# Kernel optimization log

Measured on AMD Instinct MI355X. Metric: run time of the kernel, lower is better.

Reference implementation:

```python
import jax, jax.numpy as jnp
import numpy as np

EMB = 64
L = 2
NU = 100000
NI = 50000
ER = 1000000
ET = 800000
EP = 200000


def setup_inputs() -> dict:
    key = jax.random.key(0)
    ks = jax.random.split(key, 32)
    f = jnp.float32
    def nrm(k, shape, s=0.01):
        return (jax.random.normal(k, shape) * s).astype(f)
    inp = {}
    # graph structure (int)
    inp['rate_src'] = jax.random.randint(ks[0], (ER,), 0, NU)
    inp['rate_dst'] = jax.random.randint(ks[1], (ER,), 0, NI)
    inp['trust_src'] = jax.random.randint(ks[2], (ET,), 0, NU)
    inp['trust_dst'] = jax.random.randint(ks[3], (ET,), 0, NU)
    inp['pos_u'] = jax.random.randint(ks[4], (EP,), 0, NU)
    inp['pos_i'] = jax.random.randint(ks[5], (EP,), 0, NI)
    inp['neg_u'] = jax.random.randint(ks[6], (EP,), 0, NU)
    inp['neg_i'] = jax.random.randint(ks[7], (EP,), 0, NI)
    # embeddings (init normal(0, 0.01) per init_weights)
    inp['eu'] = nrm(ks[8], (NU, EMB))
    inp['ei'] = nrm(ks[9], (NI, EMB))
    # per-rel GATv2 params, stacked over L layers; [:,0]=fc_src, [:,1]=fc_dst
    inp['rate_W'] = nrm(ks[10], (L, 2, EMB, EMB))
    inp['rate_b'] = jnp.zeros((L, 2, EMB), f)
    inp['rate_attn'] = nrm(ks[11], (L, EMB), 0.1)
    inp['rate_bias'] = jnp.zeros((L, EMB), f)
    inp['rb_W'] = nrm(ks[12], (L, 2, EMB, EMB))
    inp['rb_b'] = jnp.zeros((L, 2, EMB), f)
    inp['rb_attn'] = nrm(ks[13], (L, EMB), 0.1)
    inp['rb_bias'] = jnp.zeros((L, EMB), f)
    inp['tr_W'] = nrm(ks[14], (L, 2, EMB, EMB))
    inp['tr_b'] = jnp.zeros((L, 2, EMB), f)
    inp['tr_attn'] = nrm(ks[15], (L, EMB), 0.1)
    inp['tr_bias'] = jnp.zeros((L, EMB), f)
    # attention-gate MLPs: [:, 0]=influence, [:, 1]=interest
    inp['attW1'] = nrm(ks[16], (L, 2, 2 * EMB, 2 * EMB))
    inp['attb1'] = jnp.zeros((L, 2, 2 * EMB), f)
    inp['attW2'] = nrm(ks[17], (L, 2, 2 * EMB))
    inp['attb2'] = jnp.zeros((L, 2), f)
    return inp


def gatv2(hs, hd, src, dst, Ws, bs, Wd, bd, attn, bias, n_dst):
    # DGL GATv2Conv, num_heads=1: e = attn . leaky_relu(Ws h_u + Wd h_v), slope 0.2
    fs = hs @ Ws + bs          # [Ns, E]
    fd = hd @ Wd + bd          # [Nd, E]
    e = jax.nn.leaky_relu(fs[src] + fd[dst], 0.2) @ attn  # [E]
    m = jax.ops.segment_max(e, dst, num_segments=n_dst)
    ex = jnp.exp(e - m[dst])
    denom = jax.ops.segment_sum(ex, dst, num_segments=n_dst)
    alpha = ex / denom[dst]
    out = jax.ops.segment_sum(alpha[:, None] * fs[src], dst, num_segments=n_dst)
    return out + bias


def _bn1(x):
    # BatchNorm1d(1), training-mode batch stats, affine identity at init
    mu = jnp.mean(x)
    var = jnp.mean((x - mu) ** 2)
    return (x - mu) * jax.lax.rsqrt(var + 1e-5)


def reference(eu, ei, rate_W, rate_b, rate_attn, rate_bias, rb_W, rb_b, rb_attn,
              rb_bias, tr_W, tr_b, tr_attn, tr_bias, attW1, attb1, attW2, attb2,
              rate_src, rate_dst, trust_src, trust_dst, pos_u, pos_i, neg_u, neg_i):
    n_users, n_items = eu.shape[0], ei.shape[0]
    hu, hi = eu, ei
    res_u, res_i = [eu], [ei]
    for l in range(rate_W.shape[0]):
        # interest diffusion: rate (user->item) and rated-by (item->user, reverse edges)
        hi_new = gatv2(hu, hi, rate_src, rate_dst, rate_W[l, 0], rate_b[l, 0],
                       rate_W[l, 1], rate_b[l, 1], rate_attn[l], rate_bias[l], n_items) + hi
        q = gatv2(hi, hu, rate_dst, rate_src, rb_W[l, 0], rb_b[l, 0],
                  rb_W[l, 1], rb_b[l, 1], rb_attn[l], rb_bias[l], n_users)
        # influence diffusion: trust (user->user)
        p = gatv2(hu, hu, trust_src, trust_dst, tr_W[l, 0], tr_b[l, 0],
                  tr_W[l, 1], tr_b[l, 1], tr_attn[l], tr_bias[l], n_users)
        def att(h2, i):
            z = (h2 @ attW1[l, i] + attb1[l, i]) @ attW2[l, i] + attb2[l, i]  # [N]
            return jax.nn.leaky_relu(_bn1(z), 0.01)
        a_inf = att(jnp.concatenate([hu, p], axis=1), 0)
        a_int = att(jnp.concatenate([hu, q], axis=1), 1)
        gamma = jax.nn.softmax(jnp.stack([a_inf, a_int], axis=1), axis=1)  # [N,2]
        hu = gamma[:, 0:1] * p + gamma[:, 1:2] * q + hu
        hi = hi_new
        res_u.append(hu)
        res_i.append(hi)
    hu_all = jnp.concatenate(res_u, axis=1)  # [NU, EMB*(1+L)]
    hi_all = jnp.concatenate(res_i, axis=1)
    pos = jnp.sum(hu_all[pos_u] * hi_all[pos_i], axis=1, keepdims=True)  # [EP,1]
    neg = jnp.sum(hu_all[neg_u] * hi_all[neg_i], axis=1, keepdims=True)
    return pos, neg
```

## Files before the change

kernel.cpp:

```cpp
#include <hip/hip_runtime.h>
#include <hip/hip_bf16.h>
#include <cstdint>

typedef __hip_bfloat16 bf16;
typedef __attribute__((ext_vector_type(8))) short frag_ab;
typedef __attribute__((ext_vector_type(4))) float frag_cd;
typedef __attribute__((ext_vector_type(4))) short short4v;

__device__ __forceinline__ float b2f(short s){
  return __uint_as_float(((unsigned)(unsigned short)s) << 16);
}
__device__ __forceinline__ void bf_split(float x, short& hi, short& lo){
  bf16 h = __float2bfloat16(x);
  float hf = __bfloat162float(h);
  bf16 l = __float2bfloat16(x - hf);
  __builtin_memcpy(&hi, &h, 2);
  __builtin_memcpy(&lo, &l, 2);
}

__device__ __forceinline__ float wave_sum(float v){
#pragma unroll
  for (int o = 32; o > 0; o >>= 1) v += __shfl_down(v, o, 64);
  return v;
}

__global__ void k_copy_in(const float* __restrict__ src, float* __restrict__ dst,
                          int n, int stride){
  int idx = blockIdx.x * 256 + threadIdx.x;
  if (idx >= n * 64) return;
  int r = idx >> 6, j = idx & 63;
  dst[(size_t)r * stride + j] = src[idx];
}

__global__ void k_wsplit(const float* __restrict__ rateW, const float* __restrict__ rbW,
                         const float* __restrict__ trW,
                         short* __restrict__ Whi, short* __restrict__ Wlo){
  int tid = blockIdx.x * 256 + threadIdx.x;
  if (tid >= 12 * 4096) return;
  int m = tid >> 12, rem = tid & 4095;
  int lane = rem >> 6, rem2 = rem & 63;
  int pair = rem2 >> 3, j = rem2 & 7;
  int c = pair >> 1, h = pair & 1;
  int rel = m >> 2, li = m & 3;
  const float* base = (rel == 0) ? rateW : (rel == 1) ? rbW : trW;
  float v = base[(size_t)li * 4096 + (32 * h + (lane >> 4) * 8 + j) * 64 + 16 * c + (lane & 15)];
  short sh, sl; bf_split(v, sh, sl);
  Whi[tid] = sh; Wlo[tid] = sl;
}

__global__ void k_linear_multi(const float* __restrict__ x, int xs, int xo, int n,
                               const short* __restrict__ Whi, const short* __restrict__ Wlo,
                               int mcount,
                               int m0, const float* __restrict__ b0, bf16* __restrict__ o0,
                               int m1, const float* __restrict__ b1, bf16* __restrict__ o1,
                               int m2, const float* __restrict__ b2, bf16* __restrict__ o2,
                               int m3, const float* __restrict__ b3, bf16* __restrict__ o3){
  int lane = threadIdx.x & 63, w = threadIdx.x >> 6;
  int quad = lane >> 4, n16 = lane & 15;
  int rowbase = blockIdx.x * 64 + w * 16;
  if (rowbase >= n) return;
  int lrow = rowbase + n16; if (lrow >= n) lrow = n - 1;
  const float* xp = x + (size_t)lrow * xs + xo;
  frag_ab ahi[2], alo[2];
#pragma unroll
  for (int h = 0; h < 2; ++h){
    frag_ab vh, vl;
#pragma unroll
    for (int j = 0; j < 8; ++j){
      float xv = xp[32 * h + quad * 8 + j];
      short sh, sl; bf_split(xv, sh, sl);
      vh[j] = sh; vl[j] = sl;
    }
    ahi[h] = vh; alo[h] = vl;
  }
  int ms[4] = {m0, m1, m2, m3};
  const float* bs[4] = {b0, b1, b2, b3};
  bf16* os[4] = {o0, o1, o2, o3};
  for (int i = 0; i < mcount; ++i){
    const frag_ab* Bh = (const frag_ab*)(Whi + (size_t)ms[i] * 4096 + lane * 64);
    const frag_ab* Bl = (const frag_ab*)(Wlo + (size_t)ms[i] * 4096 + lane * 64);
    frag_cd acc[4];
#pragma unroll
    for (int c = 0; c < 4; ++c) acc[c] = frag_cd{0.f, 0.f, 0.f, 0.f};
#pragma unroll
    for (int c = 0; c < 4; ++c)
#pragma unroll
      for (int h = 0; h < 2; ++h){
        frag_ab bh = Bh[c * 2 + h], bl = Bl[c * 2 + h];
        acc[c] = __builtin_amdgcn_mfma_f32_16x16x32_bf16(ahi[h], bh, acc[c], 0, 0, 0);
        acc[c] = __builtin_amdgcn_mfma_f32_16x16x32_bf16(alo[h], bh, acc[c], 0, 0, 0);
        acc[c] = __builtin_amdgcn_mfma_f32_16x16x32_bf16(ahi[h], bl, acc[c], 0, 0, 0);
      }
    const float* bb = bs[i];
    bf16* oo = os[i];
#pragma unroll
    for (int reg = 0; reg < 4; ++reg){
      int r = rowbase + quad * 4 + reg;
      if (r >= n) continue;
#pragma unroll
      for (int c = 0; c < 4; ++c)
        oo[(size_t)r * 64 + 16 * c + n16] = __float2bfloat16(acc[c][reg] + bb[16 * c + n16]);
    }
  }
}

__global__ void k_hist2pos(const int* __restrict__ src, const int* __restrict__ dst,
                           int* __restrict__ cntA, int* __restrict__ cntB,
                           int* __restrict__ posA, int* __restrict__ posB, int E){
  int k = blockIdx.x * 256 + threadIdx.x;
  if (k >= E) return;
  posA[k] = atomicAdd(cntA + dst[k], 1);
  posB[k] = atomicAdd(cntB + src[k], 1);
}
__global__ void k_histpos(const int* __restrict__ dst, int* __restrict__ cnt,
                          int* __restrict__ pos, int E){
  int k = blockIdx.x * 256 + threadIdx.x;
  if (k >= E) return;
  pos[k] = atomicAdd(cnt + dst[k], 1);
}

__global__ void k_scan_mb(const int* __restrict__ cnt, int n,
                          int* __restrict__ offs, int* __restrict__ gbase){
  __shared__ int wsum[16];
  __shared__ int base_sh;
  int t = threadIdx.x, lane = t & 63, w = t >> 6;
  int i = blockIdx.x * 1024 + t;
  int v = (i < n) ? cnt[i] : 0;
  int x = v;
#pragma unroll
  for (int o = 1; o < 64; o <<= 1){
    int y = __shfl_up(x, o, 64);
    if (lane >= o) x += y;
  }
  if (lane == 63) wsum[w] = x;
  __syncthreads();
  if (t == 0){
    int tot = 0;
    for (int k = 0; k < 16; ++k){ int c = wsum[k]; wsum[k] = tot; tot += c; }
    base_sh = atomicAdd(gbase, tot);
  }
  __syncthreads();
  if (i < n) offs[i] = base_sh + wsum[w] + x - v;
}

__global__ void k_fill2_na(const int* __restrict__ src, const int* __restrict__ dst,
                           const int* __restrict__ offsA, const int* __restrict__ posA,
                           int* __restrict__ csrA,
                           const int* __restrict__ offsB, const int* __restrict__ posB,
                           int* __restrict__ csrB, int E){
  int t = blockIdx.x * 256 + threadIdx.x;
  int T = gridDim.x * 256;
  int k0 = t, k1 = t + T;
  bool b0 = k0 < E, b1 = k1 < E;
  int s0 = 0, d0 = 0, s1 = 0, d1 = 0, p0 = 0, q0 = 0, p1 = 0, q1 = 0;
  if (b0){ s0 = src[k0]; d0 = dst[k0]; p0 = posA[k0]; q0 = posB[k0]; }
  if (b1){ s1 = src[k1]; d1 = dst[k1]; p1 = posA[k1]; q1 = posB[k1]; }
  int oa0 = 0, ob0 = 0, oa1 = 0, ob1 = 0;
  if (b0){ oa0 = offsA[d0]; ob0 = offsB[s0]; }
  if (b1){ oa1 = offsA[d1]; ob1 = offsB[s1]; }
  if (b0){ csrA[oa0 + p0] = s0; csrB[ob0 + q0] = d0; }
  if (b1){ csrA[oa1 + p1] = s1; csrB[ob1 + q1] = d1; }
}
__global__ void k_fill_na(const int* __restrict__ src, const int* __restrict__ dst,
                          const int* __restrict__ offs, const int* __restrict__ pos,
                          int* __restrict__ csr, int E){
  int t = blockIdx.x * 256 + threadIdx.x;
  int T = gridDim.x * 256;
  int k0 = t, k1 = t + T;
  bool b0 = k0 < E, b1 = k1 < E;
  int s0 = 0, d0 = 0, p0 = 0, s1 = 0, d1 = 0, p1 = 0;
  if (b0){ s0 = src[k0]; d0 = dst[k0]; p0 = pos[k0]; }
  if (b1){ s1 = src[k1]; d1 = dst[k1]; p1 = pos[k1]; }
  int o0 = 0, o1 = 0;
  if (b0) o0 = offs[d0];
  if (b1) o1 = offs[d1];
  if (b0) csr[o0 + p0] = s0;
  if (b1) csr[o1 + p1] = s1;
}

__global__ void k_gat(const int* __restrict__ offs, const int* __restrict__ cnt,
                      const int* __restrict__ csr_src,
                      const bf16* __restrict__ fs, const bf16* __restrict__ fd,
                      const float* __restrict__ attn, const float* __restrict__ bias,
                      float* __restrict__ out, int os, int oo,
                      const float* __restrict__ res, int rs, int ro, int n){
  int d = blockIdx.x * 4 + (threadIdx.x >> 6);
  if (d >= n) return;
  int lane = threadIdx.x & 63;
  int g = lane >> 4, l16 = lane & 15;
  short4v dv = *(const short4v*)(fd + (size_t)d * 64 + 4 * l16);
  float fd0 = b2f(dv[0]), fd1 = b2f(dv[1]), fd2 = b2f(dv[2]), fd3 = b2f(dv[3]);
  float4 a4 = *(const float4*)(attn + 4 * l16);
  float acc0 = 0.f, acc1 = 0.f, acc2 = 0.f, acc3 = 0.f, den = 0.f;
  int idx0 = offs[d], end = idx0 + cnt[d];
  for (int idx = idx0; idx < end; idx += 4){
    int e = idx + g;
    bool valid = e < end;
    int s = csr_src[valid ? e : idx];
    short4v sv = *(const short4v*)(fs + (size_t)s * 64 + 4 * l16);
    float f0 = b2f(sv[0]), f1 = b2f(sv[1]), f2 = b2f(sv[2]), f3 = b2f(sv[3]);
    float v0 = f0 + fd0; v0 = (v0 > 0.f ? v0 : 0.2f * v0) * a4.x;
    float v1 = f1 + fd1; v1 = (v1 > 0.f ? v1 : 0.2f * v1) * a4.y;
    float v2 = f2 + fd2; v2 = (v2 > 0.f ? v2 : 0.2f * v2) * a4.z;
    float v3 = f3 + fd3; v3 = (v3 > 0.f ? v3 : 0.2f * v3) * a4.w;
    float tt = (v0 + v1) + (v2 + v3);
#pragma unroll
    for (int o = 1; o < 16; o <<= 1) tt += __shfl_xor(tt, o, 64);
    float ex = valid ? __expf(tt) : 0.f;
    acc0 += ex * f0; acc1 += ex * f1; acc2 += ex * f2; acc3 += ex * f3;
    den += ex;
  }
#pragma unroll
  for (int o = 16; o < 64; o <<= 1){
    acc0 += __shfl_xor(acc0, o, 64); acc1 += __shfl_xor(acc1, o, 64);
    acc2 += __shfl_xor(acc2, o, 64); acc3 += __shfl_xor(acc3, o, 64);
    den  += __shfl_xor(den, o, 64);
  }
  if (g == 0){
    float4 b4 = *(const float4*)(bias + 4 * l16);
    float inv = (den > 0.f) ? 1.f / den : 0.f;
    float o0 = acc0 * inv + b4.x, o1 = acc1 * inv + b4.y;
    float o2 = acc2 * inv + b4.z, o3 = acc3 * inv + b4.w;
    if (res){
      float4 r4 = *(const float4*)(res + (size_t)d * rs + ro + 4 * l16);
      o0 += r4.x; o1 += r4.y; o2 += r4.z; o3 += r4.w;
    }
    *(float4*)(out + (size_t)d * os + oo + 4 * l16) = make_float4(o0, o1, o2, o3);
  }
}

__global__ void k_attvec(const float* __restrict__ W1, const float* __restrict__ b1,
                         const float* __restrict__ W2, const float* __restrict__ b2,
                         float* __restrict__ vvec, float* __restrict__ cs){
  int t = threadIdx.x;
  int li = t >> 7, r = t & 127;
  float acc = 0.f;
  for (int c = 0; c < 128; ++c)
    acc += W1[(size_t)(li * 128 + r) * 128 + c] * W2[li * 128 + c];
  vvec[li * 128 + r] = acc;
  if (r == 0){
    float cacc = b2[li];
    for (int c = 0; c < 128; ++c)
      cacc += b1[li * 128 + c] * W2[li * 128 + c];
    cs[li] = cacc;
  }
}

__global__ void k_gate_z(const float* __restrict__ hu_all, int l,
                         const float* __restrict__ p, const float* __restrict__ q,
                         const float* __restrict__ vvec, const float* __restrict__ cs,
                         float* __restrict__ z1, float* __restrict__ z2,
                         float* __restrict__ bsums, int n){
  __shared__ float part[4][4];
  int w = threadIdx.x >> 6, j = threadIdx.x & 63;
  int nidx = blockIdx.x * 4 + w;
  float lz1 = 0.f, lz2 = 0.f;
  if (nidx < n){
    const float* v1 = vvec + l * 256;
    const float* v2 = vvec + l * 256 + 128;
    float h  = hu_all[(size_t)nidx * 192 + l * 64 + j];
    float pv = p[(size_t)nidx * 64 + j];
    float qv = q[(size_t)nidx * 64 + j];
    float t1 = wave_sum(h * v1[j] + pv * v1[64 + j]);
    float t2 = wave_sum(h * v2[j] + qv * v2[64 + j]);
    if (j == 0){
      lz1 = t1 + cs[l * 2 + 0];
      lz2 = t2 + cs[l * 2 + 1];
      z1[nidx] = lz1;
      z2[nidx] = lz2;
    }
  }
  if (j == 0){
    part[w][0] = lz1; part[w][1] = lz1 * lz1;
    part[w][2] = lz2; part[w][3] = lz2 * lz2;
  }
  __syncthreads();
  if (threadIdx.x < 4)
    bsums[(size_t)blockIdx.x * 4 + threadIdx.x] =
        part[0][threadIdx.x] + part[1][threadIdx.x] +
        part[2][threadIdx.x] + part[3][threadIdx.x];
}

__global__ void k_bn_part(const float* __restrict__ bsums, int nb,
                          double* __restrict__ gpart){
  __shared__ double sh[256];
  int c = threadIdx.x & 3, r0 = blockIdx.x * 64 + (threadIdx.x >> 2);
  double acc = 0.0;
  for (int i = r0; i < nb; i += gridDim.x * 64)
    acc += (double)bsums[(size_t)i * 4 + c];
  sh[threadIdx.x] = acc;
  __syncthreads();
  for (int s = 128; s >= 4; s >>= 1){
    if (threadIdx.x < s) sh[threadIdx.x] += sh[threadIdx.x + s];
    __syncthreads();
  }
  if (threadIdx.x < 4) gpart[(size_t)blockIdx.x * 4 + threadIdx.x] = sh[threadIdx.x];
}

__global__ void k_bn_final(const double* __restrict__ gpart, int nbk,
                           double* __restrict__ sums){
  __shared__ double sh[256];
  int c = threadIdx.x & 3, k0 = threadIdx.x >> 2;
  double acc = 0.0;
  for (int i = k0; i < nbk; i += 64) acc += gpart[(size_t)i * 4 + c];
  sh[threadIdx.x] = acc;
  __syncthreads();
  for (int s = 128; s >= 4; s >>= 1){
    if (threadIdx.x < s) sh[threadIdx.x] += sh[threadIdx.x + s];
    __syncthreads();
  }
  if (threadIdx.x < 4) sums[threadIdx.x] = sh[threadIdx.x];
}

__global__ void k_gate_combine(float* __restrict__ hu_all, int l,
                               const float* __restrict__ p, const float* __restrict__ q,
                               const float* __restrict__ z1, const float* __restrict__ z2,
                               const double* __restrict__ sums, int n){
  int idx = blockIdx.x * 256 + threadIdx.x;
  if (idx >= n * 64) return;
  int r = idx >> 6, j = idx & 63;
  double invn = 1.0 / (double)n;
  double mu1 = sums[0] * invn, mu2 = sums[2] * invn;
  float var1 = (float)(sums[1] * invn - mu1 * mu1);
  float var2 = (float)(sums[3] * invn - mu2 * mu2);
  float rs1 = rsqrtf(var1 + 1e-5f), rs2 = rsqrtf(var2 + 1e-5f);
  float a1 = (z1[r] - (float)mu1) * rs1;
  float a2 = (z2[r] - (float)mu2) * rs2;
  a1 = a1 > 0.f ? a1 : 0.01f * a1;
  a2 = a2 > 0.f ? a2 : 0.01f * a2;
  float mx = fmaxf(a1, a2);
  float e1 = __expf(a1 - mx), e2 = __expf(a2 - mx);
  float inv = 1.f / (e1 + e2);
  float out = (e1 * inv) * p[idx] + (e2 * inv) * q[idx]
            + hu_all[(size_t)r * 192 + l * 64 + j];
  hu_all[(size_t)r * 192 + (l + 1) * 64 + j] = out;
}

__global__ void k_score(const int* __restrict__ pu, const int* __restrict__ pi,
                        const int* __restrict__ nu, const int* __restrict__ ni,
                        const float* __restrict__ hu_all, const float* __restrict__ hi_all,
                        float* __restrict__ out, int EP){
  int gw = blockIdx.x * 4 + (threadIdx.x >> 6);
  int sub = (threadIdx.x >> 4) & 3, l16 = threadIdx.x & 15;
  int k = gw * 4 + sub;
  if (k >= 2 * EP) return;
  int u, i;
  if (k < EP){ u = pu[k]; i = pi[k]; } else { u = nu[k - EP]; i = ni[k - EP]; }
  const float4* hu = (const float4*)(hu_all + (size_t)u * 192);
  const float4* hi = (const float4*)(hi_all + (size_t)i * 192);
  float acc = 0.f;
#pragma unroll
  for (int t = 0; t < 3; ++t){
    float4 a = hu[l16 + 16 * t];
    float4 b = hi[l16 + 16 * t];
    acc += a.x * b.x + a.y * b.y + a.z * b.z + a.w * b.w;
  }
#pragma unroll
  for (int o = 8; o > 0; o >>= 1) acc += __shfl_xor(acc, o, 64);
  if (l16 == 0) out[k] = acc;
}

extern "C" void kernel_launch(void* const* d_in, const int* in_sizes, int n_in,
                              void* d_out, int out_size, void* d_ws, size_t ws_size,
                              hipStream_t stream) {
  const int*   rate_src  = (const int*)  d_in[0];
  const int*   rate_dst  = (const int*)  d_in[1];
  const int*   trust_src = (const int*)  d_in[2];
  const int*   trust_dst = (const int*)  d_in[3];
  const int*   pos_u     = (const int*)  d_in[4];
  const int*   pos_i     = (const int*)  d_in[5];
  const int*   neg_u     = (const int*)  d_in[6];
  const int*   neg_i     = (const int*)  d_in[7];
  const float* eu        = (const float*)d_in[8];
  const float* ei        = (const float*)d_in[9];
  const float* rate_W    = (const float*)d_in[10];
  const float* rate_b    = (const float*)d_in[11];
  const float* rate_attn = (const float*)d_in[12];
  const float* rate_bias = (const float*)d_in[13];
  const float* rb_W      = (const float*)d_in[14];
  const float* rb_b      = (const float*)d_in[15];
  const float* rb_attn   = (const float*)d_in[16];
  const float* rb_bias   = (const float*)d_in[17];
  const float* tr_W      = (const float*)d_in[18];
  const float* tr_b      = (const float*)d_in[19];
  const float* tr_attn   = (const float*)d_in[20];
  const float* tr_bias   = (const float*)d_in[21];
  const float* attW1     = (const float*)d_in[22];
  const float* attb1     = (const float*)d_in[23];
  const float* attW2     = (const float*)d_in[24];
  const float* attb2     = (const float*)d_in[25];

  const int ER = in_sizes[0];
  const int ET = in_sizes[2];
  const int EP = in_sizes[4];
  const int NU = in_sizes[8] / 64;
  const int NI = in_sizes[9] / 64;

  float* ws = (float*)d_ws;
  float*  hu_all = ws;
  float*  hi_all = hu_all + (size_t)NU * 192;
  float*  p      = hi_all + (size_t)NI * 192;
  float*  q      = p + (size_t)NU * 64;
  bf16*   tb     = (bf16*)(q + (size_t)NU * 64);
  bf16*   fsA    = tb;
  bf16*   fdB    = tb + (size_t)NU * 64;
  bf16*   fsC    = tb + (size_t)NU * 128;
  bf16*   fdC    = tb + (size_t)NU * 192;
  bf16*   fdA    = (bf16*)p;
  bf16*   fsB    = (bf16*)p + (size_t)NI * 64;
  int*    posA   = (int*)fsA;
  int*    posB   = (int*)fdB;
  int*    posC   = (int*)fsC;
  float*  z1     = (float*)(tb + (size_t)NU * 256);
  float*  z2     = z1 + NU;
  float*  bsums  = z2 + NU;
  float*  vvec   = bsums + (size_t)(((NU + 3) / 4) * 4);
  float*  cs     = vvec + 512;
  double* sums   = (double*)(((uintptr_t)(cs + 4) + 15) & ~(uintptr_t)15);
  double* gpart  = sums + 4;
  short*  Whi    = (short*)(gpart + 512);
  short*  Wlo    = Whi + 12 * 4096;
  int*    iw     = (int*)(Wlo + 12 * 4096);
  int*    cntA   = iw;
  int*    cntB   = cntA + NI;
  int*    cntC   = cntB + NU;
  int*    gbase  = cntC + NU;
  int*    offsA  = gbase + 4;
  int*    offsB  = offsA + NI;
  int*    offsC  = offsB + NU;
  int*    csrA   = offsC + NU;
  int*    csrB   = csrA + ER;
  int*    csrC   = csrB + ER;

  auto cdiv = [](int a, int b){ return (a + b - 1) / b; };
  const int nbz = cdiv(NU, 4);

  k_copy_in<<<cdiv(NU * 64, 256), 256, 0, stream>>>(eu, hu_all, NU, 192);
  k_copy_in<<<cdiv(NI * 64, 256), 256, 0, stream>>>(ei, hi_all, NI, 192);
  k_attvec<<<1, 512, 0, stream>>>(attW1, attb1, attW2, attb2, vvec, cs);
  k_wsplit<<<192, 256, 0, stream>>>(rate_W, rb_W, tr_W, Whi, Wlo);

  hipMemsetAsync(cntA, 0, (size_t)(NI + 2 * NU + 4) * 4, stream);
  k_hist2pos<<<cdiv(ER, 256), 256, 0, stream>>>(rate_src, rate_dst, cntA, cntB,
                                                posA, posB, ER);
  k_histpos<<<cdiv(ET, 256), 256, 0, stream>>>(trust_dst, cntC, posC, ET);
  k_scan_mb<<<cdiv(NI, 1024), 1024, 0, stream>>>(cntA, NI, offsA, gbase + 0);
  k_scan_mb<<<cdiv(NU, 1024), 1024, 0, stream>>>(cntB, NU, offsB, gbase + 1);
  k_scan_mb<<<cdiv(NU, 1024), 1024, 0, stream>>>(cntC, NU, offsC, gbase + 2);
  k_fill2_na<<<cdiv(ER, 512), 256, 0, stream>>>(rate_src, rate_dst,
      offsA, posA, csrA, offsB, posB, csrB, ER);
  k_fill_na<<<cdiv(ET, 512), 256, 0, stream>>>(trust_src, trust_dst,
      offsC, posC, csrC, ET);

  for (int l = 0; l < 2; ++l){
    k_linear_multi<<<cdiv(NU, 64), 256, 0, stream>>>(hu_all, 192, l * 64, NU, Whi, Wlo, 4,
        0 + l * 2 + 0, rate_b + (l * 2 + 0) * 64, fsA,
        4 + l * 2 + 1, rb_b   + (l * 2 + 1) * 64, fdB,
        8 + l * 2 + 0, tr_b   + (l * 2 + 0) * 64, fsC,
        8 + l * 2 + 1, tr_b   + (l * 2 + 1) * 64, fdC);
    k_linear_multi<<<cdiv(NI, 64), 256, 0, stream>>>(hi_all, 192, l * 64, NI, Whi, Wlo, 2,
        0 + l * 2 + 1, rate_b + (l * 2 + 1) * 64, fdA,
        4 + l * 2 + 0, rb_b   + (l * 2 + 0) * 64, fsB,
        0, (const float*)nullptr, (bf16*)nullptr,
        0, (const float*)nullptr, (bf16*)nullptr);

    k_gat<<<cdiv(NI, 4), 256, 0, stream>>>(offsA, cntA, csrA, fsA, fdA,
        rate_attn + l * 64, rate_bias + l * 64,
        hi_all, 192, (l + 1) * 64, hi_all, 192, l * 64, NI);
    k_gat<<<cdiv(NU, 4), 256, 0, stream>>>(offsB, cntB, csrB, fsB, fdB,
        rb_attn + l * 64, rb_bias + l * 64,
        q, 64, 0, (const float*)nullptr, 0, 0, NU);
    k_gat<<<cdiv(NU, 4), 256, 0, stream>>>(offsC, cntC, csrC, fsC, fdC,
        tr_attn + l * 64, tr_bias + l * 64,
        p, 64, 0, (const float*)nullptr, 0, 0, NU);

    k_gate_z<<<nbz, 256, 0, stream>>>(hu_all, l, p, q, vvec, cs, z1, z2, bsums, NU);
    k_bn_part<<<128, 256, 0, stream>>>(bsums, nbz, gpart);
    k_bn_final<<<1, 256, 0, stream>>>(gpart, 128, sums);
    k_gate_combine<<<cdiv(NU * 64, 256), 256, 0, stream>>>(hu_all, l, p, q, z1, z2, sums, NU);
  }

  k_score<<<cdiv(2 * EP, 16), 256, 0, stream>>>(pos_u, pos_i, neg_u, neg_i,
      hu_all, hi_all, (float*)d_out, EP);
}
```

Before: 1.001 ms.

## Add fp16 shadow embeddings for scoring, fuse graph build kernels, widen GAT lanes

Keeps fp16 copies of the user and item layer embeddings, written alongside the fp32 outputs, so the final scoring gather reads half the bytes. Merges the histogram and CSR fill kernels across relations, with positions stored as u16. Widens the GAT kernel to 8 lanes per edge with 16-byte loads, so 8 edges are processed per iteration. Risks fp16 precision loss in the scores, u16 overflow if a node's degree exceeds 65535, and needs extra workspace, falling back to fp32 when it is too small.

Measured after the change: 961.2 us. 4.0% less time.

```diff
diff --git a/kernel.cpp b/kernel.cpp
--- a/kernel.cpp
+++ b/kernel.cpp
@@ -1,14 +1,24 @@
 #include <hip/hip_runtime.h>
 #include <hip/hip_bf16.h>
+#include <hip/hip_fp16.h>
 #include <cstdint>
 
 typedef __hip_bfloat16 bf16;
 typedef __attribute__((ext_vector_type(8))) short frag_ab;
 typedef __attribute__((ext_vector_type(4))) float frag_cd;
 typedef __attribute__((ext_vector_type(4))) short short4v;
+typedef __attribute__((ext_vector_type(8))) short short8v;
+typedef unsigned short u16;
 
 __device__ __forceinline__ float b2f(short s){
   return __uint_as_float(((unsigned)(unsigned short)s) << 16);
+}
+__device__ __forceinline__ float h2f(short s){
+  __half h; __builtin_memcpy(&h, &s, 2); return __half2float(h);
+}
+__device__ __forceinline__ short f2h_s(float x){
+  __half h = __float2half(x);
+  short s; __builtin_memcpy(&s, &h, 2); return s;
 }
 __device__ __forceinline__ void bf_split(float x, short& hi, short& lo){
   bf16 h = __float2bfloat16(x);
@@ -24,12 +34,23 @@
   return v;
 }
 
-__global__ void k_copy_in(const float* __restrict__ src, float* __restrict__ dst,
-                          int n, int stride){
+__global__ void k_copy_in2(const float* __restrict__ eu, const float* __restrict__ ei,
+                           float* __restrict__ hu, float* __restrict__ hi,
+                           __half* __restrict__ huf, __half* __restrict__ hif,
+                           int NU, int NI){
   int idx = blockIdx.x * 256 + threadIdx.x;
-  if (idx >= n * 64) return;
-  int r = idx >> 6, j = idx & 63;
-  dst[(size_t)r * stride + j] = src[idx];
+  int tu = NU * 16;
+  if (idx >= tu + NI * 16) return;
+  const float* srcp; float* dstp; __half* fp_; int r, jj;
+  if (idx < tu){ r = idx >> 4; jj = idx & 15; srcp = eu; dstp = hu; fp_ = huf; }
+  else { int t = idx - tu; r = t >> 4; jj = t & 15; srcp = ei; dstp = hi; fp_ = hif; }
+  float4 v = *(const float4*)(srcp + (size_t)r * 64 + 4 * jj);
+  *(float4*)(dstp + (size_t)r * 192 + 4 * jj) = v;
+  if (fp_){
+    short4v h;
+    h[0] = f2h_s(v.x); h[1] = f2h_s(v.y); h[2] = f2h_s(v.z); h[3] = f2h_s(v.w);
+    *(short4v*)((short*)fp_ + (size_t)r * 192 + 4 * jj) = h;
+  }
 }
 
 __global__ void k_wsplit(const float* __restrict__ rateW, const float* __restrict__ rbW,
@@ -104,19 +125,21 @@
   }
 }
 
-__global__ void k_hist2pos(const int* __restrict__ src, const int* __restrict__ dst,
+__global__ void k_hist_all(const int* __restrict__ rate_src, const int* __restrict__ rate_dst,
+                           const int* __restrict__ trust_dst,
                            int* __restrict__ cntA, int* __restrict__ cntB,
-                           int* __restrict__ posA, int* __restrict__ posB, int E){
+                           int* __restrict__ cntC,
+                           u16* __restrict__ posA, u16* __restrict__ posB,
+                           u16* __restrict__ posC, int ER, int ET){
   int k = blockIdx.x * 256 + threadIdx.x;
-  if (k >= E) return;
-  posA[k] = atomicAdd(cntA + dst[k], 1);
-  posB[k] = atomicAdd(cntB + src[k], 1);
-}
-__global__ void k_histpos(const int* __restrict__ dst, int* __restrict__ cnt,
-                          int* __restrict__ pos, int E){
-  int k = blockIdx.x * 256 + threadIdx.x;
-  if (k >= E) return;
-  pos[k] = atomicAdd(cnt + dst[k], 1);
+  if (k < ER){
+    int d = rate_dst[k], s = rate_src[k];
+    posA[k] = (u16)atomicAdd(cntA + d, 1);
+    posB[k] = (u16)atomicAdd(cntB + s, 1);
+  }
+  if (k < ET){
+    posC[k] = (u16)atomicAdd(cntC + trust_dst[k], 1);
+  }
 }
 
 __global__ void k_scan_mb(const int* __restrict__ cnt, int n,
@@ -143,39 +166,24 @@
   if (i < n) offs[i] = base_sh + wsum[w] + x - v;
 }
 
-__global__ void k_fill2_na(const int* __restrict__ src, const int* __restrict__ dst,
-                           const int* __restrict__ offsA, const int* __restrict__ posA,
+__global__ void k_fill_all(const int* __restrict__ rate_src, const int* __restrict__ rate_dst,
+                           const int* __restrict__ trust_src, const int* __restrict__ trust_dst,
+                           const int* __restrict__ offsA, const u16* __restrict__ posA,
                            int* __restrict__ csrA,
-                           const int* __restrict__ offsB, const int* __restrict__ posB,
-                           int* __restrict__ csrB, int E){
-  int t = blockIdx.x * 256 + threadIdx.x;
-  int T = gridDim.x * 256;
-  int k0 = t, k1 = t + T;
-  bool b0 = k0 < E, b1 = k1 < E;
-  int s0 = 0, d0 = 0, s1 = 0, d1 = 0, p0 = 0, q0 = 0, p1 = 0, q1 = 0;
-  if (b0){ s0 = src[k0]; d0 = dst[k0]; p0 = posA[k0]; q0 = posB[k0]; }
-  if (b1){ s1 = src[k1]; d1 = dst[k1]; p1 = posA[k1]; q1 = posB[k1]; }
-  int oa0 = 0, ob0 = 0, oa1 = 0, ob1 = 0;
-  if (b0){ oa0 = offsA[d0]; ob0 = offsB[s0]; }
-  if (b1){ oa1 = offsA[d1]; ob1 = offsB[s1]; }
-  if (b0){ csrA[oa0 + p0] = s0; csrB[ob0 + q0] = d0; }
-  if (b1){ csrA[oa1 + p1] = s1; csrB[ob1 + q1] = d1; }
-}
-__global__ void k_fill_na(const int* __restrict__ src, const int* __restrict__ dst,
-                          const int* __restrict__ offs, const int* __restrict__ pos,
-                          int* __restrict__ csr, int E){
-  int t = blockIdx.x * 256 + threadIdx.x;
-  int T = gridDim.x * 256;
-  int k0 = t, k1 = t + T;
-  bool b0 = k0 < E, b1 = k1 < E;
-  int s0 = 0, d0 = 0, p0 = 0, s1 = 0, d1 = 0, p1 = 0;
-  if (b0){ s0 = src[k0]; d0 = dst[k0]; p0 = pos[k0]; }
-  if (b1){ s1 = src[k1]; d1 = dst[k1]; p1 = pos[k1]; }
-  int o0 = 0, o1 = 0;
-  if (b0) o0 = offs[d0];
-  if (b1) o1 = offs[d1];
-  if (b0) csr[o0 + p0] = s0;
-  if (b1) csr[o1 + p1] = s1;
+                           const int* __restrict__ offsB, const u16* __restrict__ posB,
+                           int* __restrict__ csrB,
+                           const int* __restrict__ offsC, const u16* __restrict__ posC,
+                           int* __restrict__ csrC, int ER, int ET){
+  int k = blockIdx.x * 256 + threadIdx.x;
+  if (k < ER){
+    int s = rate_src[k], d = rate_dst[k];
+    csrA[offsA[d] + (int)posA[k]] = s;
+    csrB[offsB[s] + (int)posB[k]] = d;
+  }
+  if (k < ET){
+    int s = trust_src[k], d = trust_dst[k];
+    csrC[offsC[d] + (int)posC[k]] = s;
+  }
 }
 
 __global__ void k_gat(const int* __restrict__ offs, const int* __restrict__ cnt,
@@ -183,49 +191,74 @@
                       const bf16* __restrict__ fs, const bf16* __restrict__ fd,
                       const float* __restrict__ attn, const float* __restrict__ bias,
                       float* __restrict__ out, int os, int oo,
-                      const float* __restrict__ res, int rs, int ro, int n){
+                      const float* __restrict__ res, int rs, int ro,
+                      __half* __restrict__ fout, int n){
   int d = blockIdx.x * 4 + (threadIdx.x >> 6);
   if (d >= n) return;
   int lane = threadIdx.x & 63;
-  int g = lane >> 4, l16 = lane & 15;
-  short4v dv = *(const short4v*)(fd + (size_t)d * 64 + 4 * l16);
-  float fd0 = b2f(dv[0]), fd1 = b2f(dv[1]), fd2 = b2f(dv[2]), fd3 = b2f(dv[3]);
-  float4 a4 = *(const float4*)(attn + 4 * l16);
-  float acc0 = 0.f, acc1 = 0.f, acc2 = 0.f, acc3 = 0.f, den = 0.f;
+  int g = lane >> 3, l8 = lane & 7;
+  short8v dv = *(const short8v*)(fd + (size_t)d * 64 + 8 * l8);
+  float fdv[8];
+#pragma unroll
+  for (int j = 0; j < 8; ++j) fdv[j] = b2f(dv[j]);
+  float4 a0 = *(const float4*)(attn + 8 * l8);
+  float4 a1 = *(const float4*)(attn + 8 * l8 + 4);
+  float a8[8] = {a0.x, a0.y, a0.z, a0.w, a1.x, a1.y, a1.z, a1.w};
+  float acc[8];
+#pragma unroll
+  for (int j = 0; j < 8; ++j) acc[j] = 0.f;
+  float den = 0.f;
   int idx0 = offs[d], end = idx0 + cnt[d];
-  for (int idx = idx0; idx < end; idx += 4){
+  for (int idx = idx0; idx < end; idx += 8){
     int e = idx + g;
     bool valid = e < end;
     int s = csr_src[valid ? e : idx];
-    short4v sv = *(const short4v*)(fs + (size_t)s * 64 + 4 * l16);
-    float f0 = b2f(sv[0]), f1 = b2f(sv[1]), f2 = b2f(sv[2]), f3 = b2f(sv[3]);
-    float v0 = f0 + fd0; v0 = (v0 > 0.f ? v0 : 0.2f * v0) * a4.x;
-    float v1 = f1 + fd1; v1 = (v1 > 0.f ? v1 : 0.2f * v1) * a4.y;
-    float v2 = f2 + fd2; v2 = (v2 > 0.f ? v2 : 0.2f * v2) * a4.z;
-    float v3 = f3 + fd3; v3 = (v3 > 0.f ? v3 : 0.2f * v3) * a4.w;
-    float tt = (v0 + v1) + (v2 + v3);
-#pragma unroll
-    for (int o = 1; o < 16; o <<= 1) tt += __shfl_xor(tt, o, 64);
+    short8v sv = *(const short8v*)(fs + (size_t)s * 64 + 8 * l8);
+    float f[8];
+    float tt = 0.f;
+#pragma unroll
+    for (int j = 0; j < 8; ++j){
+      f[j] = b2f(sv[j]);
+      float v = f[j] + fdv[j];
+      v = (v > 0.f) ? v : 0.2f * v;
+      tt += v * a8[j];
+    }
+#pragma unroll
+    for (int o = 1; o < 8; o <<= 1) tt += __shfl_xor(tt, o, 64);
     float ex = valid ? __expf(tt) : 0.f;
-    acc0 += ex * f0; acc1 += ex * f1; acc2 += ex * f2; acc3 += ex * f3;
+#pragma unroll
+    for (int j = 0; j < 8; ++j) acc[j] += ex * f[j];
     den += ex;
   }
 #pragma unroll
-  for (int o = 16; o < 64; o <<= 1){
-    acc0 += __shfl_xor(acc0, o, 64); acc1 += __shfl_xor(acc1, o, 64);
-    acc2 += __shfl_xor(acc2, o, 64); acc3 += __shfl_xor(acc3, o, 64);
-    den  += __shfl_xor(den, o, 64);
+  for (int o = 8; o < 64; o <<= 1){
+#pragma unroll
+    for (int j = 0; j < 8; ++j) acc[j] += __shfl_xor(acc[j], o, 64);
+    den += __shfl_xor(den, o, 64);
   }
   if (g == 0){
-    float4 b4 = *(const float4*)(bias + 4 * l16);
     float inv = (den > 0.f) ? 1.f / den : 0.f;
-    float o0 = acc0 * inv + b4.x, o1 = acc1 * inv + b4.y;
-    float o2 = acc2 * inv + b4.z, o3 = acc3 * inv + b4.w;
+    float4 b0 = *(const float4*)(bias + 8 * l8);
+    float4 b1 = *(const float4*)(bias + 8 * l8 + 4);
+    float o8[8];
+    o8[0] = acc[0] * inv + b0.x; o8[1] = acc[1] * inv + b0.y;
+    o8[2] = acc[2] * inv + b0.z; o8[3] = acc[3] * inv + b0.w;
+    o8[4] = acc[4] * inv + b1.x; o8[5] = acc[5] * inv + b1.y;
+    o8[6] = acc[6] * inv + b1.z; o8[7] = acc[7] * inv + b1.w;
     if (res){
-      float4 r4 = *(const float4*)(res + (size_t)d * rs + ro + 4 * l16);
-      o0 += r4.x; o1 += r4.y; o2 += r4.z; o3 += r4.w;
+      float4 r0 = *(const float4*)(res + (size_t)d * rs + ro + 8 * l8);
+      float4 r1 = *(const float4*)(res + (size_t)d * rs + ro + 8 * l8 + 4);
+      o8[0] += r0.x; o8[1] += r0.y; o8[2] += r0.z; o8[3] += r0.w;
+      o8[4] += r1.x; o8[5] += r1.y; o8[6] += r1.z; o8[7] += r1.w;
     }
-    *(float4*)(out + (size_t)d * os + oo + 4 * l16) = make_float4(o0, o1, o2, o3);
+    *(float4*)(out + (size_t)d * os + oo + 8 * l8) = make_float4(o8[0], o8[1], o8[2], o8[3]);
+    *(float4*)(out + (size_t)d * os + oo + 8 * l8 + 4) = make_float4(o8[4], o8[5], o8[6], o8[7]);
+    if (fout){
+      short8v hv;
+#pragma unroll
+      for (int j = 0; j < 8; ++j) hv[j] = f2h_s(o8[j]);
+      *(short8v*)((short*)fout + (size_t)d * 192 + 8 * l8) = hv;
+    }
   }
 }
 
@@ -315,7 +348,8 @@
 __global__ void k_gate_combine(float* __restrict__ hu_all, int l,
                                const float* __restrict__ p, const float* __restrict__ q,
                                const float* __restrict__ z1, const float* __restrict__ z2,
-                               const double* __restrict__ sums, int n){
+                               const double* __restrict__ sums,
+                               __half* __restrict__ fout, int wf32, int n){
   int idx = blockIdx.x * 256 + threadIdx.x;
   if (idx >= n * 64) return;
   int r = idx >> 6, j = idx & 63;
@@ -333,7 +367,33 @@
   float inv = 1.f / (e1 + e2);
   float out = (e1 * inv) * p[idx] + (e2 * inv) * q[idx]
             + hu_all[(size_t)r * 192 + l * 64 + j];
-  hu_all[(size_t)r * 192 + (l + 1) * 64 + j] = out;
+  if (wf32) hu_all[(size_t)r * 192 + (l + 1) * 64 + j] = out;
+  if (fout) *((short*)fout + (size_t)r * 192 + j) = f2h_s(out);
+}
+
+__global__ void k_score_f16(const int* __restrict__ pu, const int* __restrict__ pi,
+                            const int* __restrict__ nu, const int* __restrict__ ni,
+                            const __half* __restrict__ huf, const __half* __restrict__ hif,
+                            float* __restrict__ out, int EP){
+  int wv = threadIdx.x >> 6, lane = threadIdx.x & 63;
+  int g = lane >> 3, l8 = lane & 7;
+  int k = (blockIdx.x * 4 + wv) * 8 + g;
+  if (k >= 2 * EP) return;
+  int u, i;
+  if (k < EP){ u = pu[k]; i = pi[k]; } else { u = nu[k - EP]; i = ni[k - EP]; }
+  const short8v* hu = (const short8v*)(huf + (size_t)u * 192);
+  const short8v* hi = (const short8v*)(hif + (size_t)i * 192);
+  float acc = 0.f;
+#pragma unroll
+  for (int t = 0; t < 3; ++t){
+    short8v a = hu[l8 + 8 * t];
+    short8v b = hi[l8 + 8 * t];
+#pragma unroll
+    for (int j = 0; j < 8; ++j) acc += h2f(a[j]) * h2f(b[j]);
+  }
+#pragma unroll
+  for (int o = 1; o < 8; o <<= 1) acc += __shfl_xor(acc, o, 64);
+  if (l8 == 0) out[k] = acc;
 }
 
 __global__ void k_score(const int* __restrict__ pu, const int* __restrict__ pi,
@@ -395,6 +455,7 @@
   const int EP = in_sizes[4];
   const int NU = in_sizes[8] / 64;
   const int NI = in_sizes[9] / 64;
+  const int EM = (ER > ET) ? ER : ET;
 
   float* ws = (float*)d_ws;
   float*  hu_all = ws;
@@ -408,9 +469,9 @@
   bf16*   fdC    = tb + (size_t)NU * 192;
   bf16*   fdA    = (bf16*)p;
   bf16*   fsB    = (bf16*)p + (size_t)NI * 64;
-  int*    posA   = (int*)fsA;
-  int*    posB   = (int*)fdB;
-  int*    posC   = (int*)fsC;
+  u16*    posA   = (u16*)fsA;
+  u16*    posB   = (u16*)fdB;
+  u16*    posC   = (u16*)fsC;
   float*  z1     = (float*)(tb + (size_t)NU * 256);
   float*  z2     = z1 + NU;
   float*  bsums  = z2 + NU;
@@ -431,26 +492,28 @@
   int*    csrA   = offsC + NU;
   int*    csrB   = csrA + ER;
   int*    csrC   = csrB + ER;
+  uintptr_t fp16base = ((uintptr_t)(csrC + ET) + 15) & ~(uintptr_t)15;
+  __half* huf = (__half*)fp16base;
+  __half* hif = huf + (size_t)NU * 192;
+  size_t need = (uintptr_t)(hif + (size_t)NI * 192) - (uintptr_t)d_ws;
+  bool use_f16 = (need <= ws_size);
 
   auto cdiv = [](int a, int b){ return (a + b - 1) / b; };
   const int nbz = cdiv(NU, 4);
 
-  k_copy_in<<<cdiv(NU * 64, 256), 256, 0, stream>>>(eu, hu_all, NU, 192);
-  k_copy_in<<<cdiv(NI * 64, 256), 256, 0, stream>>>(ei, hi_all, NI, 192);
+  k_copy_in2<<<cdiv((NU + NI) * 16, 256), 256, 0, stream>>>(eu, ei, hu_all, hi_all,
+      use_f16 ? huf : (__half*)nullptr, use_f16 ? hif : (__half*)nullptr, NU, NI);
   k_attvec<<<1, 512, 0, stream>>>(attW1, attb1, attW2, attb2, vvec, cs);
   k_wsplit<<<192, 256, 0, stream>>>(rate_W, rb_W, tr_W, Whi, Wlo);
 
   hipMemsetAsync(cntA, 0, (size_t)(NI + 2 * NU + 4) * 4, stream);
-  k_hist2pos<<<cdiv(ER, 256), 256, 0, stream>>>(rate_src, rate_dst, cntA, cntB,
-                                                posA, posB, ER);
-  k_histpos<<<cdiv(ET, 256), 256, 0, stream>>>(trust_dst, cntC, posC, ET);
+  k_hist_all<<<cdiv(EM, 256), 256, 0, stream>>>(rate_src, rate_dst, trust_dst,
+      cntA, cntB, cntC, posA, posB, posC, ER, ET);
   k_scan_mb<<<cdiv(NI, 1024), 1024, 0, stream>>>(cntA, NI, offsA, gbase + 0);
   k_scan_mb<<<cdiv(NU, 1024), 1024, 0, stream>>>(cntB, NU, offsB, gbase + 1);
   k_scan_mb<<<cdiv(NU, 1024), 1024, 0, stream>>>(cntC, NU, offsC, gbase + 2);
-  k_fill2_na<<<cdiv(ER, 512), 256, 0, stream>>>(rate_src, rate_dst,
-      offsA, posA, csrA, offsB, posB, csrB, ER);
-  k_fill_na<<<cdiv(ET, 512), 256, 0, stream>>>(trust_src, trust_dst,
-      offsC, posC, csrC, ET);
+  k_fill_all<<<cdiv(EM, 256), 256, 0, stream>>>(rate_src, rate_dst, trust_src, trust_dst,
+      offsA, posA, csrA, offsB, posB, csrB, offsC, posC, csrC, ER, ET);
 
   for (int l = 0; l < 2; ++l){
     k_linear_multi<<<cdiv(NU, 64), 256, 0, stream>>>(hu_all, 192, l * 64, NU, Whi, Wlo, 4,
@@ -466,20 +529,27 @@
 
     k_gat<<<cdiv(NI, 4), 256, 0, stream>>>(offsA, cntA, csrA, fsA, fdA,
         rate_attn + l * 64, rate_bias + l * 64,
-        hi_all, 192, (l + 1) * 64, hi_all, 192, l * 64, NI);
+        hi_all, 192, (l + 1) * 64, hi_all, 192, l * 64,
+        use_f16 ? (hif + (size_t)(l + 1) * 64) : (__half*)nullptr, NI);
     k_gat<<<cdiv(NU, 4), 256, 0, stream>>>(offsB, cntB, csrB, fsB, fdB,
         rb_attn + l * 64, rb_bias + l * 64,
-        q, 64, 0, (const float*)nullptr, 0, 0, NU);
+        q, 64, 0, (const float*)nullptr, 0, 0, (__half*)nullptr, NU);
     k_gat<<<cdiv(NU, 4), 256, 0, stream>>>(offsC, cntC, csrC, fsC, fdC,
         tr_attn + l * 64, tr_bias + l * 64,
-        p, 64, 0, (const float*)nullptr, 0, 0, NU);
+        p, 64, 0, (const float*)nullptr, 0, 0, (__half*)nullptr, NU);
 
     k_gate_z<<<nbz, 256, 0, stream>>>(hu_all, l, p, q, vvec, cs, z1, z2, bsums, NU);
     k_bn_part<<<128, 256, 0, stream>>>(bsums, nbz, gpart);
     k_bn_final<<<1, 256, 0, stream>>>(gpart, 128, sums);
-    k_gate_combine<<<cdiv(NU * 64, 256), 256, 0, stream>>>(hu_all, l, p, q, z1, z2, sums, NU);
-  }
-
-  k_score<<<cdiv(2 * EP, 16), 256, 0, stream>>>(pos_u, pos_i, neg_u, neg_i,
-      hu_all, hi_all, (float*)d_out, EP);
-}
+    int wf32 = (!use_f16 || l == 0) ? 1 : 0;
+    k_gate_combine<<<cdiv(NU * 64, 256), 256, 0, stream>>>(hu_all, l, p, q, z1, z2, sums,
+        use_f16 ? (huf + (size_t)(l + 1) * 64) : (__half*)nullptr, wf32, NU);
+  }
+
+  if (use_f16)
+    k_score_f16<<<cdiv(2 * EP, 32), 256, 0, stream>>>(pos_u, pos_i, neg_u, neg_i,
+        huf, hif, (float*)d_out, EP);
+  else
+    k_score<<<cdiv(2 * EP, 16), 256, 0, stream>>>(pos_u, pos_i, neg_u, neg_i,
+        hu_all, hi_all, (float*)d_out, EP);
+}
```
